# Performance work log

Measured on AMD Instinct MI355X. Metric: run time of the kernel, lower is better.

Reference implementation:

```python
import jax, jax.numpy as jnp
import numpy as np

B, C, H, W = 4, 64, 128, 128
G, K, PAD, DIL = 4, 3, 2, 2  # deformable conv config
OFF_CH = 2 * K * K * G  # 72


def conv2d(x, w, b, pad):
    out = jax.lax.conv_general_dilated(
        x, w, window_strides=(1, 1), padding=[(pad, pad), (pad, pad)],
        dimension_numbers=('NCHW', 'OIHW', 'NCHW'))
    return out + b[None, :, None, None]


def deform_conv(x, offset, w, b):
    # DCNv1 (no modulation mask), groups=G, offset_groups=G, torchvision semantics.
    Bn, Cn, Hn, Wn = x.shape
    Cg = Cn // G
    Cout = w.shape[0]
    Coutg = Cout // G
    # offset channels laid out as [G, K*K, (dy,dx)]
    off = offset.reshape(Bn, G, K * K, 2, Hn, Wn)
    dy, dx = off[:, :, :, 0], off[:, :, :, 1]  # [B,G,9,H,W]
    kk = jnp.arange(K * K)
    gy = (jnp.arange(Hn)[None, :] - PAD + DIL * (kk // K)[:, None]).astype(x.dtype)[:, :, None]  # [9,H,1]
    gx = (jnp.arange(Wn)[None, :] - PAD + DIL * (kk % K)[:, None]).astype(x.dtype)[:, None, :]   # [9,1,W]
    py = dy + gy[None, None]  # [B,G,9,H,W]
    px = dx + gx[None, None]
    xg = x.reshape(Bn, G, Cg, Hn, Wn)

    def gather(img, py_, px_):  # img [Cg,H,W]; py_,px_ [9,H,W]
        y0 = jnp.floor(py_)
        x0 = jnp.floor(px_)
        ly = py_ - y0
        lx = px_ - x0

        def corner(iy, ix, wgt):
            valid = (iy >= 0) & (iy <= Hn - 1) & (ix >= 0) & (ix <= Wn - 1)
            iyc = jnp.clip(iy, 0, Hn - 1).astype(jnp.int32)
            ixc = jnp.clip(ix, 0, Wn - 1).astype(jnp.int32)
            return img[:, iyc, ixc] * (wgt * valid)[None]

        return (corner(y0, x0, (1 - ly) * (1 - lx))
                + corner(y0, x0 + 1, (1 - ly) * lx)
                + corner(y0 + 1, x0, ly * (1 - lx))
                + corner(y0 + 1, x0 + 1, ly * lx))

    sampled = jax.vmap(jax.vmap(gather))(xg, py, px)  # [B,G,Cg,9,H,W]
    wr = w.reshape(G, Coutg, Cg, K * K)
    out = jnp.einsum('bgckhw,gock->bgohw', sampled, wr).reshape(Bn, Cout, Hn, Wn)
    return out + b[None, :, None, None]


def setup_inputs() -> dict:
    key = jax.random.key(0)
    ks = jax.random.split(key, 32)
    f32 = jnp.float32
    d = {
        'Fref': jax.random.normal(ks[0], (B, C, H, W), f32),
        'Fmov1': jax.random.normal(ks[1], (B, C, H, W), f32),
        'Fmov2': jax.random.normal(ks[2], (B, C, H, W), f32),
        'cr_w': jax.random.normal(ks[3], (64, 128, 3, 3), f32) * 0.05,
        'cr_b': jax.random.normal(ks[4], (64,), f32) * 0.05,
    }
    i = 5
    for name in ('off1', 'off2', 'off3', 'off4'):
        d[name + '_w'] = jax.random.normal(ks[i], (OFF_CH, 64, 3, 3), f32) * 0.01
        d[name + '_b'] = jax.random.normal(ks[i + 1], (OFF_CH,), f32) * 0.01
        i += 2
    for name in ('d1', 'd2', 'd3', 'd4'):
        d[name + '_w'] = jax.random.normal(ks[i], (64, 64 // G, 3, 3), f32) * 0.05
        d[name + '_b'] = jax.random.normal(ks[i + 1], (64,), f32) * 0.05
        i += 2
    return d


def reference(Fref, Fmov1, Fmov2, cr_w, cr_b,
              off1_w, off1_b, off2_w, off2_b, off3_w, off3_b, off4_w, off4_b,
              d1_w, d1_b, d2_w, d2_b, d3_w, d3_b, d4_w, d4_b):
    def align(fr, fm):
        fea = conv2d(jnp.concatenate([fr, fm], axis=1), cr_w, cr_b, 1)
        fea = deform_conv(fea, conv2d(fea, off1_w, off1_b, 1), d1_w, d1_b)
        fea = deform_conv(fea, conv2d(fea, off2_w, off2_b, 1), d2_w, d2_b)
        off3 = conv2d(fea, off3_w, off3_b, 1)
        fea = deform_conv(fm, off3, d3_w, d3_b)  # note: deform3 applied to Fmov, per source
        out = deform_conv(fea, conv2d(fea, off4_w, off4_b, 1), d4_w, d4_b)
        return out

    return (align(Fref, Fmov1), align(Fref, Fmov2))
```

## Files before the change

kernel.cpp:

```cpp
#include <hip/hip_runtime.h>


using f16   = _Float16;
using f16x8 = __attribute__((ext_vector_type(8))) f16;
using h2    = __attribute__((ext_vector_type(2))) f16;
using u16x8 = __attribute__((ext_vector_type(8))) unsigned short;
using f32x4 = __attribute__((ext_vector_type(4))) float;

static constexpr int Hh = 128, Ww = 128, NB = 4, NPIX = Hh * Ww;
static constexpr int BB = 8;

__device__ __forceinline__ unsigned short f2h(float f) {
  f16 h = (f16)f;
  return *(unsigned short*)&h;
}

struct PrepPtrs {
  const float* cw[5];
  unsigned short* cd[5];
  const float* dw[4];
  unsigned short* dd[4];
  const float* ob[4];
  float* obd[4];
};

__global__ __launch_bounds__(256) void prep_all_kernel(PrepPtrs pp) {
  const int which = blockIdx.y;
  const int i = blockIdx.x * 256 + threadIdx.x;
  if (which == 0) {
    if (i >= 9 * 64 * 128) return;
    const int cin = 128, cop = 64;
    const int ci = i % cin, co = (i / cin) % cop, t = i / (cin * cop);
    pp.cd[0][i] = f2h(pp.cw[0][((size_t)co * cin + ci) * 9 + t]);
  } else if (which <= 4) {
    if (i >= 9 * 80 * 64) return;
    const int cin = 64, cop = 80;
    const int ci = i % cin, co = (i / cin) % cop, t = i / (cin * cop);
    const int g = co / 20, c = co % 20;
    float v = (c < 18) ? pp.cw[which][((size_t)(g * 18 + c) * cin + ci) * 9 + t]
                       : 0.f;
    pp.cd[which][i] = f2h(v);
  } else if (which <= 8) {
    if (i >= 4 * 5 * 16 * 32) return;
    const int kk = i & 31, o = (i >> 5) & 15, pair = (i >> 9) % 5;
    const int g = i / 2560;
    const int t = pair * 2 + (kk >> 4), c = kk & 15;
    float v = (t < 9) ? pp.dw[which - 5][(size_t)((g * 16 + o) * 16 + c) * 9 + t]
                      : 0.f;
    pp.dd[which - 5][i] = f2h(v);
  } else {
    if (i >= 4 * 80) return;
    const int ten = i / 80, co = i % 80;
    const int g = co / 20, c = co % 20;
    pp.obd[ten][co] = (c < 18) ? pp.ob[ten][g * 18 + c] : 0.f;
  }
}

__global__ __launch_bounds__(256) void to_gs_kernel(
    const float* __restrict__ Fref, const float* __restrict__ Fm1,
    const float* __restrict__ Fm2, unsigned short* __restrict__ frefG,
    unsigned short* __restrict__ fmovG) {
  const int t = blockIdx.x * 256 + threadIdx.x;
  const int b2 = t >> 14, pix = t & (NPIX - 1);
  const float* fm = (b2 < 4 ? Fm1 : Fm2) + (size_t)(b2 & 3) * 64 * NPIX + pix;
  for (int c8 = 0; c8 < 8; ++c8) {
    u16x8 v;
#pragma unroll
    for (int j = 0; j < 8; ++j) v[j] = f2h(fm[(size_t)(c8 * 8 + j) * NPIX]);
    *(u16x8*)(fmovG + ((size_t)(b2 * 4 + (c8 >> 1)) * NPIX + pix) * 16 +
              (c8 & 1) * 8) = v;
  }
  if (b2 < 4) {
    const float* fr = Fref + (size_t)b2 * 64 * NPIX + pix;
    for (int c8 = 0; c8 < 8; ++c8) {
      u16x8 v;
#pragma unroll
      for (int j = 0; j < 8; ++j) v[j] = f2h(fr[(size_t)(c8 * 8 + j) * NPIX]);
      *(u16x8*)(frefG + ((size_t)(b2 * 4 + (c8 >> 1)) * NPIX + pix) * 16 +
                (c8 & 1) * 8) = v;
    }
  }
}

template <int CIN, int COP, int CO_REAL, int OST, bool OUT_GS, bool OFF_GS>
__global__ __launch_bounds__(512, 4) void convmfma_kernel(
    const unsigned short* __restrict__ in0, int bmask0,
    const unsigned short* __restrict__ in1, int bmask1,
    const unsigned short* __restrict__ wT,
    const float* __restrict__ biasP,
    unsigned short* __restrict__ out) {
  constexpr int COF = COP / 16;
  constexpr int NCH = CIN / 64;
  constexpr int NT = NCH * 9;
  __shared__ unsigned short sW[2][COP * 64];
  __shared__ unsigned short sB[324 * 64];

  const int tile = blockIdx.x, b = blockIdx.y;
  const int ty0 = (tile >> 3) << 4, tx0 = (tile & 7) << 4;
  const int tid = threadIdx.x;
  const int wv = tid >> 6, l = tid & 63;
  const int lm = l & 15, lq = l >> 4;

  f32x4 acc[COF][2];
#pragma unroll
  for (int cf = 0; cf < COF; ++cf)
#pragma unroll
    for (int pf = 0; pf < 2; ++pf) acc[cf][pf] = (f32x4){0.f, 0.f, 0.f, 0.f};

  const unsigned short* base0 = in0 + (size_t)(b & bmask0) * 4 * NPIX * 16;
  const unsigned short* base1 =
      (NCH > 1) ? in1 + (size_t)(b & bmask1) * 4 * NPIX * 16 : nullptr;

  auto stage_input = [&](int ch) {
    const unsigned short* inB = (ch == 0) ? base0 : base1;
    for (int q = tid; q < 324 * 8; q += 512) {
      const int pix = q >> 3, ci8 = q & 7;
      const int r = pix / 18, c = pix - r * 18;
      const int gy = ty0 - 1 + r, gx = tx0 - 1 + c;
      u16x8 v;
      if (gy >= 0 && gy < Hh && gx >= 0 && gx < Ww) {
        v = *(const u16x8*)(inB + ((size_t)(ci8 >> 1) * NPIX + gy * Ww + gx) *
                                      16 + (ci8 & 1) * 8);
      } else {
#pragma unroll
        for (int j = 0; j < 8; ++j) v[j] = 0;
      }
      const int boff = pix * 128 + ((ci8 * 16) ^ ((pix & 7) << 4));
      *(u16x8*)((char*)sB + boff) = v;
    }
  };
  auto stage_w = [&](int tt, int buf) {
    const int ch = tt / 9, t = tt - ch * 9;
    for (int q = tid; q < COP * 8; q += 512) {
      const int ci8 = q & 7;
      const int co = q >> 3;
      u16x8 v = *(const u16x8*)(wT + (size_t)(t * COP + co) * CIN + ch * 64 +
                                ci8 * 8);
      const int aoff = co * 128 + ((ci8 * 16) ^ ((co & 7) << 4));
      *(u16x8*)((char*)sW[buf] + aoff) = v;
    }
  };

  stage_input(0);
  stage_w(0, 0);
  __syncthreads();

  for (int tt = 0; tt < NT; ++tt) {
    const int t = tt % 9;
    const bool nextNewCh = ((tt + 1) % 9 == 0);
    if (tt + 1 < NT && !nextNewCh) stage_w(tt + 1, (tt + 1) & 1);

    const int dy = t / 3, dx = t - dy * 3;
    const char* sWc = (const char*)sW[tt & 1];
#pragma unroll
    for (int kc = 0; kc < 2; ++kc) {
      f16x8 afr[COF];
#pragma unroll
      for (int cf = 0; cf < COF; ++cf) {
        const int co = cf * 16 + lm;
        const int aoff = co * 128 + ((kc * 64 + lq * 16) ^ ((co & 7) << 4));
        afr[cf] = *(const f16x8*)(sWc + aoff);
      }
#pragma unroll
      for (int pf = 0; pf < 2; ++pf) {
        const int pix = wv * 32 + pf * 16 + lm;
        const int spix = ((pix >> 4) + dy) * 18 + (pix & 15) + dx;
        const int boff = spix * 128 + ((kc * 64 + lq * 16) ^ ((spix & 7) << 4));
        const f16x8 bfr = *(const f16x8*)((const char*)sB + boff);
#pragma unroll
        for (int cf = 0; cf < COF; ++cf)
          acc[cf][pf] = __builtin_amdgcn_mfma_f32_16x16x32_f16(
              afr[cf], bfr, acc[cf][pf], 0, 0, 0);
      }
    }
    __syncthreads();
    if (tt + 1 < NT && nextNewCh) {
      stage_input((tt + 1) / 9);
      stage_w(tt + 1, (tt + 1) & 1);
      __syncthreads();
    }
  }

  unsigned short* outB = out + (size_t)b * NPIX * OST;
#pragma unroll
  for (int cf = 0; cf < COF; ++cf) {
    const int co0 = cf * 16 + lq * 4;
    if (co0 >= CO_REAL) continue;
    const float4 bv = *(const float4*)(biasP + co0);
#pragma unroll
    for (int pf = 0; pf < 2; ++pf) {
      const int pix = wv * 32 + pf * 16 + lm;
      const int gpix = (ty0 + (pix >> 4)) * Ww + tx0 + (pix & 15);
      const f32x4 v = acc[cf][pf];
      ushort4 pk;
      pk.x = f2h(v[0] + bv.x);
      pk.y = f2h(v[1] + bv.y);
      pk.z = f2h(v[2] + bv.z);
      pk.w = f2h(v[3] + bv.w);
      if (OUT_GS) {
        *(ushort4*)(out + ((size_t)(b * 4 + cf) * NPIX + gpix) * 16 + lq * 4) =
            pk;
      } else if (OFF_GS) {
        const int gg = co0 / 20, cc = co0 % 20;
        *(ushort4*)(out + ((size_t)(b * 4 + gg) * NPIX + gpix) * 20 + cc) = pk;
      } else {
        *(ushort4*)(outB + (size_t)gpix * OST + co0) = pk;
      }
    }
  }
}

template <bool NCHW_OUT>
__global__ __launch_bounds__(256, 4) void deform13_kernel(
    const unsigned short* __restrict__ x,
    const unsigned short* __restrict__ off,
    const unsigned short* __restrict__ dwP,
    const float* __restrict__ bias,
    float* __restrict__ outF, unsigned short* __restrict__ outH) {
  __shared__ char sB[128 * 80];
  const int tile = blockIdx.x, g = blockIdx.y, b = blockIdx.z;
  const int ty0 = (tile >> 2) << 2;
  const int tx0 = (tile & 3) << 5;
  const int tid = threadIdx.x;
  const int p = tid >> 1, h = tid & 1;
  const int l = tid & 63, wv = tid >> 6;
  const int lm = l & 15, lq = l >> 4;
  const int y = ty0 + (p >> 5), xx = tx0 + (p & 31);

  const unsigned short* xP = x + (size_t)(b * 4 + g) * NPIX * 16 + h * 8;
  const unsigned short* offP =
      off + ((size_t)(b * 4 + g) * NPIX + y * Ww + xx) * 20;

  unsigned od[9];
#pragma unroll
  for (int t = 0; t < 9; ++t) od[t] = *(const unsigned*)(offP + 2 * t);

  f16x8 afr[5];
#pragma unroll
  for (int pr = 0; pr < 5; ++pr)
    afr[pr] = *(const f16x8*)(dwP + ((size_t)(g * 5 + pr) * 16 + lm) * 32 +
                              lq * 8);

  f32x4 acc[2];
  acc[0] = (f32x4){0.f, 0.f, 0.f, 0.f};
  acc[1] = (f32x4){0.f, 0.f, 0.f, 0.f};

  char* myB = sB + p * 80 + h * 16;

#pragma unroll
  for (int pair = 0; pair < 5; ++pair) {
#pragma unroll
    for (int ti = 0; ti < 2; ++ti) {
      const int t = pair * 2 + ti;
      uint4 sv = (uint4){0u, 0u, 0u, 0u};
      if (t < 9) {
        const unsigned odw = od[t];
        const f16* op = (const f16*)&odw;
        const float dy = (float)op[0];
        const float dx = (float)op[1];
        const float py = dy + (float)(y - 2 + 2 * (t / 3));
        const float px = dx + (float)(xx - 2 + 2 * (t % 3));
        const float fy = floorf(py), fx = floorf(px);
        const int y0 = (int)fy, x0 = (int)fx;
        const int y1 = y0 + 1, x1 = x0 + 1;
        const float ly = py - fy, lx = px - fx;
        float w00 = (1.f - ly) * (1.f - lx), w01 = (1.f - ly) * lx;
        float w10 = ly * (1.f - lx), w11 = ly * lx;
        const bool vy0 = (y0 >= 0) && (y0 < Hh), vy1 = (y1 >= 0) && (y1 < Hh);
        const bool vx0 = (x0 >= 0) && (x0 < Ww), vx1 = (x1 >= 0) && (x1 < Ww);
        w00 = (vy0 && vx0) ? w00 : 0.f;
        w01 = (vy0 && vx1) ? w01 : 0.f;
        w10 = (vy1 && vx0) ? w10 : 0.f;
        w11 = (vy1 && vx1) ? w11 : 0.f;
        const int y0c = min(max(y0, 0), Hh - 1), y1c = min(max(y1, 0), Hh - 1);
        const int x0c = min(max(x0, 0), Ww - 1), x1c = min(max(x1, 0), Ww - 1);
        const u16x8 a00 = *(const u16x8*)(xP + (size_t)(y0c * Ww + x0c) * 16);
        const u16x8 a01 = *(const u16x8*)(xP + (size_t)(y0c * Ww + x1c) * 16);
        const u16x8 a10 = *(const u16x8*)(xP + (size_t)(y1c * Ww + x0c) * 16);
        const u16x8 a11 = *(const u16x8*)(xP + (size_t)(y1c * Ww + x1c) * 16);
        const h2* c00 = (const h2*)&a00;
        const h2* c01 = (const h2*)&a01;
        const h2* c10 = (const h2*)&a10;
        const h2* c11 = (const h2*)&a11;
        const f16 h00 = (f16)w00, h01 = (f16)w01;
        const f16 h10 = (f16)w10, h11 = (f16)w11;
        const h2 p00 = (h2){h00, h00}, p01 = (h2){h01, h01};
        const h2 p10 = (h2){h10, h10}, p11 = (h2){h11, h11};
        unsigned fw[4];
#pragma unroll
        for (int j = 0; j < 4; ++j) {
          h2 r = c00[j] * p00;
          r += c01[j] * p01;
          r += c10[j] * p10;
          r += c11[j] * p11;
          fw[j] = *(const unsigned*)&r;
        }
        sv = (uint4){fw[0], fw[1], fw[2], fw[3]};
      }
      *(uint4*)(myB + ti * 32) = sv;
    }
#pragma unroll
    for (int n = 0; n < 2; ++n) {
      const f16x8 bfr =
          *(const f16x8*)(sB + (wv * 32 + n * 16 + lm) * 80 + lq * 16);
      acc[n] = __builtin_amdgcn_mfma_f32_16x16x32_f16(afr[pair], bfr, acc[n],
                                                      0, 0, 0);
    }
  }

  const float4 bv = *(const float4*)(bias + g * 16 + lq * 4);
#pragma unroll
  for (int n = 0; n < 2; ++n) {
    const int pixl = wv * 32 + n * 16 + lm;
    const int gpix = (ty0 + (pixl >> 5)) * Ww + tx0 + (pixl & 31);
    const f32x4 v = acc[n];
    if (NCHW_OUT) {
      float* oB = outF + (size_t)(b * 64 + g * 16 + lq * 4) * NPIX + gpix;
      oB[0] = v[0] + bv.x;
      oB[NPIX] = v[1] + bv.y;
      oB[2 * NPIX] = v[2] + bv.z;
      oB[3 * NPIX] = v[3] + bv.w;
    } else {
      ushort4 pk;
      pk.x = f2h(v[0] + bv.x);
      pk.y = f2h(v[1] + bv.y);
      pk.z = f2h(v[2] + bv.z);
      pk.w = f2h(v[3] + bv.w);
      *(ushort4*)(outH + ((size_t)(b * 4 + g) * NPIX + gpix) * 16 + lq * 4) =
          pk;
    }
  }
}


extern "C" void kernel_launch(void* const* d_in, const int* in_sizes, int n_in,
                              void* d_out, int out_size, void* d_ws,
                              size_t ws_size, hipStream_t stream) {
  const float* Fref = (const float*)d_in[0];
  const float* Fmov1 = (const float*)d_in[1];
  const float* Fmov2 = (const float*)d_in[2];
  const float* cr_w = (const float*)d_in[3];
  const float* cr_b = (const float*)d_in[4];
  const float* offw[4] = {(const float*)d_in[5], (const float*)d_in[7],
                          (const float*)d_in[9], (const float*)d_in[11]};
  const float* offb[4] = {(const float*)d_in[6], (const float*)d_in[8],
                          (const float*)d_in[10], (const float*)d_in[12]};
  const float* dw[4] = {(const float*)d_in[13], (const float*)d_in[15],
                        (const float*)d_in[17], (const float*)d_in[19]};
  const float* db[4] = {(const float*)d_in[14], (const float*)d_in[16],
                        (const float*)d_in[18], (const float*)d_in[20]};

  char* p = (char*)d_ws;
  auto carve = [&](size_t bytes) {
    void* r = p;
    p += (bytes + 255) & ~(size_t)255;
    return r;
  };
  unsigned short* frefG = (unsigned short*)carve((size_t)4 * 4 * NPIX * 16 * 2);
  unsigned short* fmovG = (unsigned short*)carve((size_t)BB * 4 * NPIX * 16 * 2);
  unsigned short* feaA = (unsigned short*)carve((size_t)BB * 4 * NPIX * 16 * 2);
  unsigned short* feaB = (unsigned short*)carve((size_t)BB * 4 * NPIX * 16 * 2);
  unsigned short* offB = (unsigned short*)carve((size_t)BB * 4 * NPIX * 20 * 2);
  unsigned short* wcrT = (unsigned short*)carve((size_t)9 * 64 * 128 * 2);
  unsigned short* woffT[4];
  for (int i = 0; i < 4; ++i)
    woffT[i] = (unsigned short*)carve((size_t)9 * 80 * 64 * 2);
  unsigned short* dwP[4];
  for (int i = 0; i < 4; ++i)
    dwP[i] = (unsigned short*)carve((size_t)4 * 5 * 16 * 32 * 2);
  float* obP[4];
  for (int i = 0; i < 4; ++i) obP[i] = (float*)carve((size_t)80 * 4);

  PrepPtrs pp;
  pp.cw[0] = cr_w;
  pp.cd[0] = wcrT;
  for (int i = 0; i < 4; ++i) {
    pp.cw[i + 1] = offw[i];
    pp.cd[i + 1] = woffT[i];
    pp.dw[i] = dw[i];
    pp.dd[i] = dwP[i];
    pp.ob[i] = offb[i];
    pp.obd[i] = obP[i];
  }
  prep_all_kernel<<<dim3(288, 10), 256, 0, stream>>>(pp);

  to_gs_kernel<<<BB * NPIX / 256, 256, 0, stream>>>(Fref, Fmov1, Fmov2, frefG,
                                                    fmovG);

  const dim3 cgrid(64, BB), cblk(512);
  const dim3 dgrid(128, 4, BB), dblk(256);
  float* outF = (float*)d_out;

  convmfma_kernel<128, 64, 64, 0, true, false><<<cgrid, cblk, 0, stream>>>(
      frefG, 3, fmovG, 7, wcrT, cr_b, feaA);
  convmfma_kernel<64, 80, 80, 20, false, true><<<cgrid, cblk, 0, stream>>>(
      feaA, 7, nullptr, 0, woffT[0], obP[0], offB);
  deform13_kernel<false>
      <<<dgrid, dblk, 0, stream>>>(feaA, offB, dwP[0], db[0], nullptr, feaB);
  convmfma_kernel<64, 80, 80, 20, false, true><<<cgrid, cblk, 0, stream>>>(
      feaB, 7, nullptr, 0, woffT[1], obP[1], offB);
  deform13_kernel<false>
      <<<dgrid, dblk, 0, stream>>>(feaB, offB, dwP[1], db[1], nullptr, feaA);
  convmfma_kernel<64, 80, 80, 20, false, true><<<cgrid, cblk, 0, stream>>>(
      feaA, 7, nullptr, 0, woffT[2], obP[2], offB);
  deform13_kernel<false>
      <<<dgrid, dblk, 0, stream>>>(fmovG, offB, dwP[2], db[2], nullptr, feaB);
  convmfma_kernel<64, 80, 80, 20, false, true><<<cgrid, cblk, 0, stream>>>(
      feaB, 7, nullptr, 0, woffT[3], obP[3], offB);
  deform13_kernel<true>
      <<<dgrid, dblk, 0, stream>>>(feaB, offB, dwP[3], db[3], outF, nullptr);
}
```

Baseline: 257.4 us.

## Fuse offset convolution with deformable sampling conv into one kernel per stage

Each offset-prediction convolution and the deformable convolution that consumes its output now run in a single kernel. The offsets stay in LDS per 16x16 tile instead of being written to and re-read from a global offset buffer. This removes four launches and the global round-trip of the offset tensor. In exchange it uses more LDS per block (about 62KB) and lower declared occupancy. The deform stage now loops over the four groups serially in the same block, so each block has less parallel work.

```diff
diff --git a/kernel.cpp b/kernel.cpp
--- a/kernel.cpp
+++ b/kernel.cpp
@@ -82,8 +82,8 @@
   }
 }
 
-template <int CIN, int COP, int CO_REAL, int OST, bool OUT_GS, bool OFF_GS>
-__global__ __launch_bounds__(512, 4) void convmfma_kernel(
+template <int CIN, int COP, int CO_REAL>
+__global__ __launch_bounds__(512, 2) void convmfma_kernel(
     const unsigned short* __restrict__ in0, int bmask0,
     const unsigned short* __restrict__ in1, int bmask1,
     const unsigned short* __restrict__ wT,
@@ -181,7 +181,6 @@
     }
   }
 
-  unsigned short* outB = out + (size_t)b * NPIX * OST;
 #pragma unroll
   for (int cf = 0; cf < COF; ++cf) {
     const int co0 = cf * 16 + lq * 4;
@@ -197,137 +196,218 @@
       pk.y = f2h(v[1] + bv.y);
       pk.z = f2h(v[2] + bv.z);
       pk.w = f2h(v[3] + bv.w);
-      if (OUT_GS) {
-        *(ushort4*)(out + ((size_t)(b * 4 + cf) * NPIX + gpix) * 16 + lq * 4) =
-            pk;
-      } else if (OFF_GS) {
-        const int gg = co0 / 20, cc = co0 % 20;
-        *(ushort4*)(out + ((size_t)(b * 4 + gg) * NPIX + gpix) * 20 + cc) = pk;
-      } else {
-        *(ushort4*)(outB + (size_t)gpix * OST + co0) = pk;
-      }
+      const int gg = co0 >> 4, cc = co0 & 15;
+      *(ushort4*)(out + ((size_t)(b * 4 + gg) * NPIX + gpix) * 16 + cc) = pk;
     }
   }
 }
 
 template <bool NCHW_OUT>
-__global__ __launch_bounds__(256, 4) void deform13_kernel(
-    const unsigned short* __restrict__ x,
-    const unsigned short* __restrict__ off,
+__global__ __launch_bounds__(512, 2) void fused_od_kernel(
+    const unsigned short* __restrict__ convIn,
+    const unsigned short* __restrict__ sampX,
+    const unsigned short* __restrict__ wT,
+    const float* __restrict__ obias,
     const unsigned short* __restrict__ dwP,
-    const float* __restrict__ bias,
+    const float* __restrict__ dbias,
     float* __restrict__ outF, unsigned short* __restrict__ outH) {
-  __shared__ char sB[128 * 80];
-  const int tile = blockIdx.x, g = blockIdx.y, b = blockIdx.z;
-  const int ty0 = (tile >> 2) << 2;
-  const int tx0 = (tile & 3) << 5;
+  __shared__ __attribute__((aligned(16))) char lds[61952];
+  unsigned short* sB = (unsigned short*)lds;
+  char* sWr = lds + 41472;
+  char* sOffB = lds;
+  char* bounce = lds + 40960;
+
+  const int tile = blockIdx.x, b = blockIdx.y;
+  const int ty0 = (tile >> 3) << 4, tx0 = (tile & 7) << 4;
   const int tid = threadIdx.x;
-  const int p = tid >> 1, h = tid & 1;
-  const int l = tid & 63, wv = tid >> 6;
+  const int wv = tid >> 6, l = tid & 63;
   const int lm = l & 15, lq = l >> 4;
-  const int y = ty0 + (p >> 5), xx = tx0 + (p & 31);
-
-  const unsigned short* xP = x + (size_t)(b * 4 + g) * NPIX * 16 + h * 8;
-  const unsigned short* offP =
-      off + ((size_t)(b * 4 + g) * NPIX + y * Ww + xx) * 20;
-
-  unsigned od[9];
-#pragma unroll
-  for (int t = 0; t < 9; ++t) od[t] = *(const unsigned*)(offP + 2 * t);
-
-  f16x8 afr[5];
-#pragma unroll
-  for (int pr = 0; pr < 5; ++pr)
-    afr[pr] = *(const f16x8*)(dwP + ((size_t)(g * 5 + pr) * 16 + lm) * 32 +
-                              lq * 8);
-
-  f32x4 acc[2];
-  acc[0] = (f32x4){0.f, 0.f, 0.f, 0.f};
-  acc[1] = (f32x4){0.f, 0.f, 0.f, 0.f};
-
-  char* myB = sB + p * 80 + h * 16;
-
-#pragma unroll
-  for (int pair = 0; pair < 5; ++pair) {
-#pragma unroll
-    for (int ti = 0; ti < 2; ++ti) {
-      const int t = pair * 2 + ti;
-      uint4 sv = (uint4){0u, 0u, 0u, 0u};
-      if (t < 9) {
-        const unsigned odw = od[t];
-        const f16* op = (const f16*)&odw;
-        const float dy = (float)op[0];
-        const float dx = (float)op[1];
-        const float py = dy + (float)(y - 2 + 2 * (t / 3));
-        const float px = dx + (float)(xx - 2 + 2 * (t % 3));
-        const float fy = floorf(py), fx = floorf(px);
-        const int y0 = (int)fy, x0 = (int)fx;
-        const int y1 = y0 + 1, x1 = x0 + 1;
-        const float ly = py - fy, lx = px - fx;
-        float w00 = (1.f - ly) * (1.f - lx), w01 = (1.f - ly) * lx;
-        float w10 = ly * (1.f - lx), w11 = ly * lx;
-        const bool vy0 = (y0 >= 0) && (y0 < Hh), vy1 = (y1 >= 0) && (y1 < Hh);
-        const bool vx0 = (x0 >= 0) && (x0 < Ww), vx1 = (x1 >= 0) && (x1 < Ww);
-        w00 = (vy0 && vx0) ? w00 : 0.f;
-        w01 = (vy0 && vx1) ? w01 : 0.f;
-        w10 = (vy1 && vx0) ? w10 : 0.f;
-        w11 = (vy1 && vx1) ? w11 : 0.f;
-        const int y0c = min(max(y0, 0), Hh - 1), y1c = min(max(y1, 0), Hh - 1);
-        const int x0c = min(max(x0, 0), Ww - 1), x1c = min(max(x1, 0), Ww - 1);
-        const u16x8 a00 = *(const u16x8*)(xP + (size_t)(y0c * Ww + x0c) * 16);
-        const u16x8 a01 = *(const u16x8*)(xP + (size_t)(y0c * Ww + x1c) * 16);
-        const u16x8 a10 = *(const u16x8*)(xP + (size_t)(y1c * Ww + x0c) * 16);
-        const u16x8 a11 = *(const u16x8*)(xP + (size_t)(y1c * Ww + x1c) * 16);
-        const h2* c00 = (const h2*)&a00;
-        const h2* c01 = (const h2*)&a01;
-        const h2* c10 = (const h2*)&a10;
-        const h2* c11 = (const h2*)&a11;
-        const f16 h00 = (f16)w00, h01 = (f16)w01;
-        const f16 h10 = (f16)w10, h11 = (f16)w11;
-        const h2 p00 = (h2){h00, h00}, p01 = (h2){h01, h01};
-        const h2 p10 = (h2){h10, h10}, p11 = (h2){h11, h11};
-        unsigned fw[4];
-#pragma unroll
-        for (int j = 0; j < 4; ++j) {
-          h2 r = c00[j] * p00;
-          r += c01[j] * p01;
-          r += c10[j] * p10;
-          r += c11[j] * p11;
-          fw[j] = *(const unsigned*)&r;
-        }
-        sv = (uint4){fw[0], fw[1], fw[2], fw[3]};
-      }
-      *(uint4*)(myB + ti * 32) = sv;
-    }
-#pragma unroll
-    for (int n = 0; n < 2; ++n) {
-      const f16x8 bfr =
-          *(const f16x8*)(sB + (wv * 32 + n * 16 + lm) * 80 + lq * 16);
-      acc[n] = __builtin_amdgcn_mfma_f32_16x16x32_f16(afr[pair], bfr, acc[n],
-                                                      0, 0, 0);
-    }
-  }
-
-  const float4 bv = *(const float4*)(bias + g * 16 + lq * 4);
-#pragma unroll
-  for (int n = 0; n < 2; ++n) {
-    const int pixl = wv * 32 + n * 16 + lm;
-    const int gpix = (ty0 + (pixl >> 5)) * Ww + tx0 + (pixl & 31);
-    const f32x4 v = acc[n];
-    if (NCHW_OUT) {
-      float* oB = outF + (size_t)(b * 64 + g * 16 + lq * 4) * NPIX + gpix;
-      oB[0] = v[0] + bv.x;
-      oB[NPIX] = v[1] + bv.y;
-      oB[2 * NPIX] = v[2] + bv.z;
-      oB[3 * NPIX] = v[3] + bv.w;
+
+  f32x4 acc[5][2];
+#pragma unroll
+  for (int cf = 0; cf < 5; ++cf)
+#pragma unroll
+    for (int pf = 0; pf < 2; ++pf) acc[cf][pf] = (f32x4){0.f, 0.f, 0.f, 0.f};
+
+  const unsigned short* inB = convIn + (size_t)b * 4 * NPIX * 16;
+
+  for (int q = tid; q < 324 * 8; q += 512) {
+    const int pix = q >> 3, ci8 = q & 7;
+    const int r = pix / 18, c = pix - r * 18;
+    const int gy = ty0 - 1 + r, gx = tx0 - 1 + c;
+    u16x8 v;
+    if (gy >= 0 && gy < Hh && gx >= 0 && gx < Ww) {
+      v = *(const u16x8*)(inB + ((size_t)(ci8 >> 1) * NPIX + gy * Ww + gx) *
+                                    16 + (ci8 & 1) * 8);
     } else {
+#pragma unroll
+      for (int j = 0; j < 8; ++j) v[j] = 0;
+    }
+    const int boff = pix * 128 + ((ci8 * 16) ^ ((pix & 7) << 4));
+    *(u16x8*)((char*)sB + boff) = v;
+  }
+  auto stage_w = [&](int t, int buf) {
+    for (int q = tid; q < 80 * 8; q += 512) {
+      const int ci8 = q & 7;
+      const int co = q >> 3;
+      u16x8 v = *(const u16x8*)(wT + (size_t)(t * 80 + co) * 64 + ci8 * 8);
+      const int aoff = co * 128 + ((ci8 * 16) ^ ((co & 7) << 4));
+      *(u16x8*)(sWr + buf * 10240 + aoff) = v;
+    }
+  };
+  stage_w(0, 0);
+  __syncthreads();
+
+  for (int t = 0; t < 9; ++t) {
+    if (t + 1 < 9) stage_w(t + 1, (t + 1) & 1);
+    const int dy = t / 3, dx = t - dy * 3;
+    const char* sWc = sWr + (t & 1) * 10240;
+#pragma unroll
+    for (int kc = 0; kc < 2; ++kc) {
+      f16x8 afr[5];
+#pragma unroll
+      for (int cf = 0; cf < 5; ++cf) {
+        const int co = cf * 16 + lm;
+        const int aoff = co * 128 + ((kc * 64 + lq * 16) ^ ((co & 7) << 4));
+        afr[cf] = *(const f16x8*)(sWc + aoff);
+      }
+#pragma unroll
+      for (int pf = 0; pf < 2; ++pf) {
+        const int pix = wv * 32 + pf * 16 + lm;
+        const int spix = ((pix >> 4) + dy) * 18 + (pix & 15) + dx;
+        const int boff = spix * 128 + ((kc * 64 + lq * 16) ^ ((spix & 7) << 4));
+        const f16x8 bfr = *(const f16x8*)((const char*)sB + boff);
+#pragma unroll
+        for (int cf = 0; cf < 5; ++cf)
+          acc[cf][pf] = __builtin_amdgcn_mfma_f32_16x16x32_f16(
+              afr[cf], bfr, acc[cf][pf], 0, 0, 0);
+      }
+    }
+    __syncthreads();
+  }
+
+#pragma unroll
+  for (int cf = 0; cf < 5; ++cf) {
+    const int co0 = cf * 16 + lq * 4;
+    const float4 bv = *(const float4*)(obias + co0);
+#pragma unroll
+    for (int pf = 0; pf < 2; ++pf) {
+      const int pix = wv * 32 + pf * 16 + lm;
+      const f32x4 v = acc[cf][pf];
       ushort4 pk;
       pk.x = f2h(v[0] + bv.x);
       pk.y = f2h(v[1] + bv.y);
       pk.z = f2h(v[2] + bv.z);
       pk.w = f2h(v[3] + bv.w);
-      *(ushort4*)(outH + ((size_t)(b * 4 + g) * NPIX + gpix) * 16 + lq * 4) =
-          pk;
+      *(ushort4*)(sOffB + pix * 160 + co0 * 2) = pk;
+    }
+  }
+  __syncthreads();
+
+  const int p = tid >> 1, h = tid & 1;
+  const int y = ty0 + (p >> 4), xx = tx0 + (p & 15);
+  char* myB = bounce + p * 80 + h * 16;
+
+  for (int g = 0; g < 4; ++g) {
+    const unsigned short* xP =
+        sampX + (size_t)(b * 4 + g) * NPIX * 16 + h * 8;
+    unsigned od[9];
+#pragma unroll
+    for (int t = 0; t < 9; ++t)
+      od[t] = *(const unsigned*)(sOffB + p * 160 + (g * 20 + 2 * t) * 2);
+
+    f16x8 afr[5];
+#pragma unroll
+    for (int pr = 0; pr < 5; ++pr)
+      afr[pr] = *(const f16x8*)(dwP + ((size_t)(g * 5 + pr) * 16 + lm) * 32 +
+                                lq * 8);
+
+    f32x4 dacc[2];
+    dacc[0] = (f32x4){0.f, 0.f, 0.f, 0.f};
+    dacc[1] = (f32x4){0.f, 0.f, 0.f, 0.f};
+
+#pragma unroll
+    for (int pair = 0; pair < 5; ++pair) {
+#pragma unroll
+      for (int ti = 0; ti < 2; ++ti) {
+        const int t = pair * 2 + ti;
+        uint4 sv = (uint4){0u, 0u, 0u, 0u};
+        if (t < 9) {
+          const unsigned odw = od[t];
+          const f16* op = (const f16*)&odw;
+          const float dy = (float)op[0];
+          const float dx = (float)op[1];
+          const float py = dy + (float)(y - 2 + 2 * (t / 3));
+          const float px = dx + (float)(xx - 2 + 2 * (t % 3));
+          const float fy = floorf(py), fx = floorf(px);
+          const int y0 = (int)fy, x0 = (int)fx;
+          const int y1 = y0 + 1, x1 = x0 + 1;
+          const float ly = py - fy, lx = px - fx;
+          float w00 = (1.f - ly) * (1.f - lx), w01 = (1.f - ly) * lx;
+          float w10 = ly * (1.f - lx), w11 = ly * lx;
+          const bool vy0 = (y0 >= 0) && (y0 < Hh), vy1 = (y1 >= 0) && (y1 < Hh);
+          const bool vx0 = (x0 >= 0) && (x0 < Ww), vx1 = (x1 >= 0) && (x1 < Ww);
+          w00 = (vy0 && vx0) ? w00 : 0.f;
+          w01 = (vy0 && vx1) ? w01 : 0.f;
+          w10 = (vy1 && vx0) ? w10 : 0.f;
+          w11 = (vy1 && vx1) ? w11 : 0.f;
+          const int y0c = min(max(y0, 0), Hh - 1), y1c = min(max(y1, 0), Hh - 1);
+          const int x0c = min(max(x0, 0), Ww - 1), x1c = min(max(x1, 0), Ww - 1);
+          const u16x8 a00 = *(const u16x8*)(xP + (size_t)(y0c * Ww + x0c) * 16);
+          const u16x8 a01 = *(const u16x8*)(xP + (size_t)(y0c * Ww + x1c) * 16);
+          const u16x8 a10 = *(const u16x8*)(xP + (size_t)(y1c * Ww + x0c) * 16);
+          const u16x8 a11 = *(const u16x8*)(xP + (size_t)(y1c * Ww + x1c) * 16);
+          const h2* c00 = (const h2*)&a00;
+          const h2* c01 = (const h2*)&a01;
+          const h2* c10 = (const h2*)&a10;
+          const h2* c11 = (const h2*)&a11;
+          const f16 h00 = (f16)w00, h01 = (f16)w01;
+          const f16 h10 = (f16)w10, h11 = (f16)w11;
+          const h2 p00 = (h2){h00, h00}, p01 = (h2){h01, h01};
+          const h2 p10 = (h2){h10, h10}, p11 = (h2){h11, h11};
+          unsigned fw[4];
+#pragma unroll
+          for (int j = 0; j < 4; ++j) {
+            h2 r = c00[j] * p00;
+            r += c01[j] * p01;
+            r += c10[j] * p10;
+            r += c11[j] * p11;
+            fw[j] = *(const unsigned*)&r;
+          }
+          sv = (uint4){fw[0], fw[1], fw[2], fw[3]};
+        }
+        *(uint4*)(myB + ti * 32) = sv;
+      }
+#pragma unroll
+      for (int n = 0; n < 2; ++n) {
+        const f16x8 bfr =
+            *(const f16x8*)(bounce + (wv * 32 + n * 16 + lm) * 80 + lq * 16);
+        dacc[n] = __builtin_amdgcn_mfma_f32_16x16x32_f16(afr[pair], bfr,
+                                                         dacc[n], 0, 0, 0);
+      }
+    }
+
+    const float4 bv = *(const float4*)(dbias + g * 16 + lq * 4);
+#pragma unroll
+    for (int n = 0; n < 2; ++n) {
+      const int pixl = wv * 32 + n * 16 + lm;
+      const int gpix = (ty0 + (pixl >> 4)) * Ww + tx0 + (pixl & 15);
+      const f32x4 v = dacc[n];
+      if (NCHW_OUT) {
+        float* oB = outF + (size_t)(b * 64 + g * 16 + lq * 4) * NPIX + gpix;
+        oB[0] = v[0] + bv.x;
+        oB[NPIX] = v[1] + bv.y;
+        oB[2 * NPIX] = v[2] + bv.z;
+        oB[3 * NPIX] = v[3] + bv.w;
+      } else {
+        ushort4 pk;
+        pk.x = f2h(v[0] + bv.x);
+        pk.y = f2h(v[1] + bv.y);
+        pk.z = f2h(v[2] + bv.z);
+        pk.w = f2h(v[3] + bv.w);
+        *(ushort4*)(outH + ((size_t)(b * 4 + g) * NPIX + gpix) * 16 + lq * 4) =
+            pk;
+      }
     }
   }
 }
@@ -360,7 +440,6 @@
   unsigned short* fmovG = (unsigned short*)carve((size_t)BB * 4 * NPIX * 16 * 2);
   unsigned short* feaA = (unsigned short*)carve((size_t)BB * 4 * NPIX * 16 * 2);
   unsigned short* feaB = (unsigned short*)carve((size_t)BB * 4 * NPIX * 16 * 2);
-  unsigned short* offB = (unsigned short*)carve((size_t)BB * 4 * NPIX * 20 * 2);
   unsigned short* wcrT = (unsigned short*)carve((size_t)9 * 64 * 128 * 2);
   unsigned short* woffT[4];
   for (int i = 0; i < 4; ++i)
@@ -387,26 +466,17 @@
   to_gs_kernel<<<BB * NPIX / 256, 256, 0, stream>>>(Fref, Fmov1, Fmov2, frefG,
                                                     fmovG);
 
-  const dim3 cgrid(64, BB), cblk(512);
-  const dim3 dgrid(128, 4, BB), dblk(256);
+  const dim3 fgrid(64, BB), fblk(512);
   float* outF = (float*)d_out;
 
-  convmfma_kernel<128, 64, 64, 0, true, false><<<cgrid, cblk, 0, stream>>>(
+  convmfma_kernel<128, 64, 64><<<fgrid, fblk, 0, stream>>>(
       frefG, 3, fmovG, 7, wcrT, cr_b, feaA);
-  convmfma_kernel<64, 80, 80, 20, false, true><<<cgrid, cblk, 0, stream>>>(
-      feaA, 7, nullptr, 0, woffT[0], obP[0], offB);
-  deform13_kernel<false>
-      <<<dgrid, dblk, 0, stream>>>(feaA, offB, dwP[0], db[0], nullptr, feaB);
-  convmfma_kernel<64, 80, 80, 20, false, true><<<cgrid, cblk, 0, stream>>>(
-      feaB, 7, nullptr, 0, woffT[1], obP[1], offB);
-  deform13_kernel<false>
-      <<<dgrid, dblk, 0, stream>>>(feaB, offB, dwP[1], db[1], nullptr, feaA);
-  convmfma_kernel<64, 80, 80, 20, false, true><<<cgrid, cblk, 0, stream>>>(
-      feaA, 7, nullptr, 0, woffT[2], obP[2], offB);
-  deform13_kernel<false>
-      <<<dgrid, dblk, 0, stream>>>(fmovG, offB, dwP[2], db[2], nullptr, feaB);
-  convmfma_kernel<64, 80, 80, 20, false, true><<<cgrid, cblk, 0, stream>>>(
-      feaB, 7, nullptr, 0, woffT[3], obP[3], offB);
-  deform13_kernel<true>
-      <<<dgrid, dblk, 0, stream>>>(feaB, offB, dwP[3], db[3], outF, nullptr);
-}
+  fused_od_kernel<false><<<fgrid, fblk, 0, stream>>>(
+      feaA, feaA, woffT[0], obP[0], dwP[0], db[0], nullptr, feaB);
+  fused_od_kernel<false><<<fgrid, fblk, 0, stream>>>(
+      feaB, feaB, woffT[1], obP[1], dwP[1], db[1], nullptr, feaA);
+  fused_od_kernel<false><<<fgrid, fblk, 0, stream>>>(
+      feaA, fmovG, woffT[2], obP[2], dwP[2], db[2], nullptr, feaB);
+  fused_od_kernel<true><<<fgrid, fblk, 0, stream>>>(
+      feaB, feaB, woffT[3], obP[3], dwP[3], db[3], outF, nullptr);
+}
```

New measurement: 239.7 us. 6.9% less time.
